# Performance work log

Hardware: AMD Instinct MI355X
Metric: run time of the kernel (lower is better)

Reference implementation:

```python
import jax, jax.numpy as jnp
import numpy as np

NUM_GROUPS = 128  # number of distinct values in min_t_idx (fixed for jit)


def _ball_volume(dim, radius):
    # dim is a static python int (NI - 1)
    if dim == 1:
        return 2.0 * radius
    if dim == 2:
        return jnp.pi * radius ** 2
    if dim == 3:
        return (4.0 / 3.0) * jnp.pi * radius ** 3
    raise ValueError(f'Only 1D-3D KDE volumes are supported, got dimension {dim}.')


def setup_inputs() -> dict:
    key = jax.random.key(0)
    k1, k2 = jax.random.split(key)
    M, NI = 16384, 3
    x = jax.random.normal(k1, (M, NI), dtype=jnp.float32)
    min_t_idx = jax.random.randint(k2, (M,), 0, NUM_GROUPS, dtype=jnp.int32)
    return {"x": x, "min_t_idx": min_t_idx, "K": 16}


def reference(x, min_t_idx, K):
    # Equivalent to the per-group python loop in the torch module, but done
    # densely: mask cross-group pairs to +inf and take the K-th smallest
    # distance per row (torch.kthvalue includes the self-distance 0, as here).
    M, NI = x.shape
    dim = NI - 1

    counts = jnp.bincount(min_t_idx, length=NUM_GROUPS)  # group sizes c
    c = counts[min_t_idx].astype(x.dtype)                # [M] size of own group (== N)

    # pairwise euclidean distances within groups
    sq = jnp.sum(x * x, axis=1)                          # [M]
    d2 = sq[:, None] + sq[None, :] - 2.0 * (x @ x.T)     # [M, M]
    dist = jnp.sqrt(jnp.maximum(d2, 0.0))
    same_group = min_t_idx[:, None] == min_t_idx[None, :]
    dist = jnp.where(same_group, dist, jnp.inf)

    # K-th smallest distance per row (includes self-distance 0)
    neg_topk, _ = jax.lax.top_k(-dist, K)                # [M, K]
    knn_dist = -neg_topk[:, K - 1]                       # [M]

    p_kde = _ball_volume(dim, knn_dist) / (K - 1)
    p_fallback = 1.0 / c                                 # groups with N < K
    p = jnp.where(c < K, p_fallback, p_kde)

    # original runs entirely under torch.no_grad()
    return jax.lax.stop_gradient(p)
```

## Files before the change

### kernel.cpp

```cpp
#include <hip/hip_runtime.h>
#include <hip/hip_bf16.h>
#include <float.h>

#define NGROUPS 128
#define SLOT    512
#define SB      512
#define RCAP    512


#define BUB(S) { const float lo_ = fminf(S, v); v = fmaxf(S, v); S = lo_; }

__global__ __launch_bounds__(SB) void kde_fused(
        const float* __restrict__ x,
        const int* __restrict__ idx,
        const int* __restrict__ Kptr,
        int M,
        float* __restrict__ out) {
    const int g = blockIdx.x >> 1;
    const int h = blockIdx.x & 1;

    __shared__ float4 cand[SLOT];
    __shared__ int    rows[RCAP];
    __shared__ float  Alds[2][64][17];
    __shared__ float  Blds[2][64][17];
    __shared__ int    lc, rc;

    const int tid  = threadIdx.x;
    const int wv   = tid >> 6;
    const int lane = tid & 63;

    if (tid == 0) { lc = 0; rc = 0; }
    __syncthreads();

    const int lo = h * (M >> 1);
    const int hi = lo + (M >> 1);

#define KDE_TRY(pid_)                                                         \
    do {                                                                      \
        const int pid = (pid_);                                               \
        int p = atomicAdd(&lc, 1);                                            \
        if (p < SLOT) {                                                       \
            float4 v;                                                         \
            v.x = x[3 * pid + 0];                                             \
            v.y = x[3 * pid + 1];                                             \
            v.z = x[3 * pid + 2];                                             \
            v.w = __int_as_float(pid);                                        \
            cand[p] = v;                                                      \
            if (pid >= lo && pid < hi) {                                      \
                int r = atomicAdd(&rc, 1);                                    \
                if (r < RCAP) rows[r] = p;                                    \
            }                                                                 \
        }                                                                     \
    } while (0)

    const int4* __restrict__ idx4 = (const int4*)idx;
    const int M4 = M >> 2;
    for (int i = tid; i < M4; i += SB) {
        const int4 v = idx4[i];
        const int base = i << 2;
        if (v.x == g) KDE_TRY(base + 0);
        if (v.y == g) KDE_TRY(base + 1);
        if (v.z == g) KDE_TRY(base + 2);
        if (v.w == g) KDE_TRY(base + 3);
    }
    for (int i = (M4 << 2) + tid; i < M; i += SB)
        if (idx[i] == g) KDE_TRY(i);
#undef KDE_TRY
    __syncthreads();

    int c  = lc;  c  = (c  < SLOT) ? c  : SLOT;
    int nr = rc;  nr = (nr < RCAP) ? nr : RCAP;
    const int K0 = Kptr[0];
    const int K  = (K0 < 16) ? K0 : 16;

    const int rg = wv >> 1;
    const int sp = wv & 1;

    const int ch = (c + 1) >> 1;
    const int j0 = sp ? ch : 0;
    const int j1 = sp ? c  : ch;

    for (int rbase = 0; rbase < nr; rbase += 128) {
        const bool grpActive = (wv < 4) && (rbase + rg * 64 < nr);
        const int  ridx      = rbase + rg * 64 + lane;
        const bool rowOK     = grpActive && (ridx < nr);
        int rslot = rowOK ? rows[ridx] : 0;
        rslot = (rslot >= 0 && rslot < SLOT) ? rslot : 0;
        const float4 rp = cand[rslot];

        float s0 = FLT_MAX, s1 = FLT_MAX, s2 = FLT_MAX, s3 = FLT_MAX;
        float s4 = FLT_MAX, s5 = FLT_MAX, s6 = FLT_MAX, s7 = FLT_MAX;
        float s8 = FLT_MAX, s9 = FLT_MAX, s10 = FLT_MAX, s11 = FLT_MAX;
        float s12 = FLT_MAX, s13 = FLT_MAX, s14 = FLT_MAX, s15 = FLT_MAX;

        if (grpActive) {
#pragma unroll 4
            for (int j = j0; j < j1; ++j) {
                const float4 q = cand[j];
                const float dx = q.x - rp.x;
                const float dy = q.y - rp.y;
                const float dz = q.z - rp.z;
                float v = dx * dx + dy * dy + dz * dz;
                BUB(s0)  BUB(s1)  BUB(s2)  BUB(s3)
                BUB(s4)  BUB(s5)  BUB(s6)  BUB(s7)
                BUB(s8)  BUB(s9)  BUB(s10) BUB(s11)
                BUB(s12) BUB(s13) BUB(s14) BUB(s15)
            }
            float (*dst)[17] = sp ? Blds[rg] : Alds[rg];
            dst[lane][0]  = s0;  dst[lane][1]  = s1;  dst[lane][2]  = s2;
            dst[lane][3]  = s3;  dst[lane][4]  = s4;  dst[lane][5]  = s5;
            dst[lane][6]  = s6;  dst[lane][7]  = s7;  dst[lane][8]  = s8;
            dst[lane][9]  = s9;  dst[lane][10] = s10; dst[lane][11] = s11;
            dst[lane][12] = s12; dst[lane][13] = s13; dst[lane][14] = s14;
            dst[lane][15] = s15;
        }
        __syncthreads();

        if (rowOK && sp == 0) {
            float kth;
            if (K == 16) {
                const float b0  = Blds[rg][lane][0],  b1  = Blds[rg][lane][1];
                const float b2  = Blds[rg][lane][2],  b3  = Blds[rg][lane][3];
                const float b4  = Blds[rg][lane][4],  b5  = Blds[rg][lane][5];
                const float b6  = Blds[rg][lane][6],  b7  = Blds[rg][lane][7];
                const float b8  = Blds[rg][lane][8],  b9  = Blds[rg][lane][9];
                const float b10 = Blds[rg][lane][10], b11 = Blds[rg][lane][11];
                const float b12 = Blds[rg][lane][12], b13 = Blds[rg][lane][13];
                const float b14 = Blds[rg][lane][14], b15 = Blds[rg][lane][15];
                float best = b15;
                best = fminf(best, fmaxf(s0,  b14));
                best = fminf(best, fmaxf(s1,  b13));
                best = fminf(best, fmaxf(s2,  b12));
                best = fminf(best, fmaxf(s3,  b11));
                best = fminf(best, fmaxf(s4,  b10));
                best = fminf(best, fmaxf(s5,  b9));
                best = fminf(best, fmaxf(s6,  b8));
                best = fminf(best, fmaxf(s7,  b7));
                best = fminf(best, fmaxf(s8,  b6));
                best = fminf(best, fmaxf(s9,  b5));
                best = fminf(best, fmaxf(s10, b4));
                best = fminf(best, fmaxf(s11, b3));
                best = fminf(best, fmaxf(s12, b2));
                best = fminf(best, fmaxf(s13, b1));
                best = fminf(best, fmaxf(s14, b0));
                best = fminf(best, s15);
                kth = best;
            } else {
                float best = FLT_MAX;
                for (int i = 0; i <= K; ++i) {
                    const float a = (i > 0)     ? Alds[rg][lane][i - 1]     : -FLT_MAX;
                    const float b = (K - i > 0) ? Blds[rg][lane][K - i - 1] : -FLT_MAX;
                    best = fminf(best, fmaxf(a, b));
                }
                kth = best;
            }
            const float pi = 3.14159265358979323846f;
            const float p = (c < K0) ? (1.0f / (float)c)
                                     : (pi * kth / (float)(K0 - 1));
            out[__float_as_int(rp.w)] = p;
        }
        __syncthreads();
    }
}

extern "C" void kernel_launch(void* const* d_in, const int* in_sizes, int n_in,
                              void* d_out, int out_size, void* d_ws, size_t ws_size,
                              hipStream_t stream) {
    const float* x   = (const float*)d_in[0];
    const int*   idx = (const int*)d_in[1];
    const int*   Kp  = (const int*)d_in[2];
    float* out = (float*)d_out;

    const int M = in_sizes[1];

    kde_fused<<<NGROUPS * 2, SB, 0, stream>>>(x, idx, Kp, M, out);
}
```

Baseline: 19.71 us.

## Split candidate scan across eight waves with bitonic tree merge of top-16 lists

Each row is now processed by all eight wavefronts, each scanning one eighth of the group's candidates, instead of two waves per row over half the candidates. The per-wave sorted top-16 lists are combined in a three-level tree through shared memory, using a bitonic min-merge so each merge stays sorted. This shortens the serial insertion-sort scan per thread, and every wave now does useful work instead of four idling. In exchange it adds three block barriers and extra merge ALU per 64-row batch, and rows are processed in batches of 64 rather than 128.

```diff
diff --git a/kernel.cpp b/kernel.cpp
--- a/kernel.cpp
+++ b/kernel.cpp
@@ -9,6 +9,7 @@
 
 
 #define BUB(S) { const float lo_ = fminf(S, v); v = fmaxf(S, v); S = lo_; }
+#define CS(a, b) { const float lo_ = fminf(a, b); b = fmaxf(a, b); a = lo_; }
 
 __global__ __launch_bounds__(SB) void kde_fused(
         const float* __restrict__ x,
@@ -21,8 +22,7 @@
 
     __shared__ float4 cand[SLOT];
     __shared__ int    rows[RCAP];
-    __shared__ float  Alds[2][64][17];
-    __shared__ float  Blds[2][64][17];
+    __shared__ float  lists[4][64][17];
     __shared__ int    lc, rc;
 
     const int tid  = threadIdx.x;
@@ -33,7 +33,7 @@
     __syncthreads();
 
     const int lo = h * (M >> 1);
-    const int hi = lo + (M >> 1);
+    const int hi = (h == 1) ? M : (M >> 1);
 
 #define KDE_TRY(pid_)                                                         \
     do {                                                                      \
@@ -71,93 +71,89 @@
     int c  = lc;  c  = (c  < SLOT) ? c  : SLOT;
     int nr = rc;  nr = (nr < RCAP) ? nr : RCAP;
     const int K0 = Kptr[0];
-    const int K  = (K0 < 16) ? K0 : 16;
 
-    const int rg = wv >> 1;
-    const int sp = wv & 1;
+    const int sh = (c + 7) >> 3;
+    const int j0 = wv * sh;
+    const int j1 = ((j0 + sh) < c) ? (j0 + sh) : c;
 
-    const int ch = (c + 1) >> 1;
-    const int j0 = sp ? ch : 0;
-    const int j1 = sp ? c  : ch;
+#define PUB(i)                                                                 \
+    do {                                                                       \
+        float* L = lists[i][lane];                                             \
+        L[0]=r0; L[1]=r1; L[2]=r2;  L[3]=r3;  L[4]=r4;  L[5]=r5;  L[6]=r6;     \
+        L[7]=r7; L[8]=r8; L[9]=r9;  L[10]=r10;L[11]=r11;L[12]=r12;L[13]=r13;   \
+        L[14]=r14; L[15]=r15;                                                  \
+    } while (0)
 
-    for (int rbase = 0; rbase < nr; rbase += 128) {
-        const bool grpActive = (wv < 4) && (rbase + rg * 64 < nr);
-        const int  ridx      = rbase + rg * 64 + lane;
-        const bool rowOK     = grpActive && (ridx < nr);
+#define MERGE16(i)                                                             \
+    do {                                                                       \
+        const float* L = lists[i][lane];                                       \
+        float m0  = fminf(r0,  L[15]); float m1  = fminf(r1,  L[14]);          \
+        float m2  = fminf(r2,  L[13]); float m3  = fminf(r3,  L[12]);          \
+        float m4  = fminf(r4,  L[11]); float m5  = fminf(r5,  L[10]);          \
+        float m6  = fminf(r6,  L[9]);  float m7  = fminf(r7,  L[8]);           \
+        float m8  = fminf(r8,  L[7]);  float m9  = fminf(r9,  L[6]);           \
+        float m10 = fminf(r10, L[5]);  float m11 = fminf(r11, L[4]);           \
+        float m12 = fminf(r12, L[3]);  float m13 = fminf(r13, L[2]);           \
+        float m14 = fminf(r14, L[1]);  float m15 = fminf(r15, L[0]);           \
+        CS(m0,m8)  CS(m1,m9)  CS(m2,m10) CS(m3,m11)                            \
+        CS(m4,m12) CS(m5,m13) CS(m6,m14) CS(m7,m15)                            \
+        CS(m0,m4)  CS(m1,m5)  CS(m2,m6)  CS(m3,m7)                             \
+        CS(m8,m12) CS(m9,m13) CS(m10,m14) CS(m11,m15)                          \
+        CS(m0,m2)  CS(m1,m3)  CS(m4,m6)  CS(m5,m7)                             \
+        CS(m8,m10) CS(m9,m11) CS(m12,m14) CS(m13,m15)                          \
+        CS(m0,m1)  CS(m2,m3)  CS(m4,m5)  CS(m6,m7)                             \
+        CS(m8,m9)  CS(m10,m11) CS(m12,m13) CS(m14,m15)                         \
+        r0=m0; r1=m1; r2=m2;  r3=m3;  r4=m4;  r5=m5;  r6=m6;  r7=m7;           \
+        r8=m8; r9=m9; r10=m10; r11=m11; r12=m12; r13=m13; r14=m14; r15=m15;    \
+    } while (0)
+
+    for (int rbase = 0; rbase < nr; rbase += 64) {
+        const int  ridx  = rbase + lane;
+        const bool rowOK = (ridx < nr);
         int rslot = rowOK ? rows[ridx] : 0;
         rslot = (rslot >= 0 && rslot < SLOT) ? rslot : 0;
         const float4 rp = cand[rslot];
 
-        float s0 = FLT_MAX, s1 = FLT_MAX, s2 = FLT_MAX, s3 = FLT_MAX;
-        float s4 = FLT_MAX, s5 = FLT_MAX, s6 = FLT_MAX, s7 = FLT_MAX;
-        float s8 = FLT_MAX, s9 = FLT_MAX, s10 = FLT_MAX, s11 = FLT_MAX;
-        float s12 = FLT_MAX, s13 = FLT_MAX, s14 = FLT_MAX, s15 = FLT_MAX;
+        float r0 = FLT_MAX, r1 = FLT_MAX, r2 = FLT_MAX, r3 = FLT_MAX;
+        float r4 = FLT_MAX, r5 = FLT_MAX, r6 = FLT_MAX, r7 = FLT_MAX;
+        float r8 = FLT_MAX, r9 = FLT_MAX, r10 = FLT_MAX, r11 = FLT_MAX;
+        float r12 = FLT_MAX, r13 = FLT_MAX, r14 = FLT_MAX, r15 = FLT_MAX;
 
-        if (grpActive) {
-#pragma unroll 4
-            for (int j = j0; j < j1; ++j) {
-                const float4 q = cand[j];
-                const float dx = q.x - rp.x;
-                const float dy = q.y - rp.y;
-                const float dz = q.z - rp.z;
-                float v = dx * dx + dy * dy + dz * dz;
-                BUB(s0)  BUB(s1)  BUB(s2)  BUB(s3)
-                BUB(s4)  BUB(s5)  BUB(s6)  BUB(s7)
-                BUB(s8)  BUB(s9)  BUB(s10) BUB(s11)
-                BUB(s12) BUB(s13) BUB(s14) BUB(s15)
+        for (int j = j0; j < j1; ++j) {
+            const float4 q = cand[j];
+            const float dx = q.x - rp.x;
+            const float dy = q.y - rp.y;
+            const float dz = q.z - rp.z;
+            float v = dx * dx + dy * dy + dz * dz;
+            BUB(r0)  BUB(r1)  BUB(r2)  BUB(r3)
+            BUB(r4)  BUB(r5)  BUB(r6)  BUB(r7)
+            BUB(r8)  BUB(r9)  BUB(r10) BUB(r11)
+            BUB(r12) BUB(r13) BUB(r14) BUB(r15)
+        }
+
+        if (wv >= 4) PUB(wv - 4);
+        __syncthreads();
+        if (wv < 4) MERGE16(wv);
+        if (wv == 2 || wv == 3) PUB(wv);
+        __syncthreads();
+        if (wv < 2) MERGE16(wv + 2);
+        if (wv == 1) PUB(1);
+        __syncthreads();
+        if (wv == 0) {
+            MERGE16(1);
+            if (rowOK) {
+                float kth;
+                if (K0 >= 16) {
+                    kth = r15;
+                } else {
+                    PUB(0);
+                    kth = lists[0][lane][K0 - 1];
+                }
+                const float pi = 3.14159265358979323846f;
+                const float p = (c < K0) ? (1.0f / (float)c)
+                                         : (pi * kth / (float)(K0 - 1));
+                out[__float_as_int(rp.w)] = p;
             }
-            float (*dst)[17] = sp ? Blds[rg] : Alds[rg];
-            dst[lane][0]  = s0;  dst[lane][1]  = s1;  dst[lane][2]  = s2;
-            dst[lane][3]  = s3;  dst[lane][4]  = s4;  dst[lane][5]  = s5;
-            dst[lane][6]  = s6;  dst[lane][7]  = s7;  dst[lane][8]  = s8;
-            dst[lane][9]  = s9;  dst[lane][10] = s10; dst[lane][11] = s11;
-            dst[lane][12] = s12; dst[lane][13] = s13; dst[lane][14] = s14;
-            dst[lane][15] = s15;
-        }
-        __syncthreads();
-
-        if (rowOK && sp == 0) {
-            float kth;
-            if (K == 16) {
-                const float b0  = Blds[rg][lane][0],  b1  = Blds[rg][lane][1];
-                const float b2  = Blds[rg][lane][2],  b3  = Blds[rg][lane][3];
-                const float b4  = Blds[rg][lane][4],  b5  = Blds[rg][lane][5];
-                const float b6  = Blds[rg][lane][6],  b7  = Blds[rg][lane][7];
-                const float b8  = Blds[rg][lane][8],  b9  = Blds[rg][lane][9];
-                const float b10 = Blds[rg][lane][10], b11 = Blds[rg][lane][11];
-                const float b12 = Blds[rg][lane][12], b13 = Blds[rg][lane][13];
-                const float b14 = Blds[rg][lane][14], b15 = Blds[rg][lane][15];
-                float best = b15;
-                best = fminf(best, fmaxf(s0,  b14));
-                best = fminf(best, fmaxf(s1,  b13));
-                best = fminf(best, fmaxf(s2,  b12));
-                best = fminf(best, fmaxf(s3,  b11));
-                best = fminf(best, fmaxf(s4,  b10));
-                best = fminf(best, fmaxf(s5,  b9));
-                best = fminf(best, fmaxf(s6,  b8));
-                best = fminf(best, fmaxf(s7,  b7));
-                best = fminf(best, fmaxf(s8,  b6));
-                best = fminf(best, fmaxf(s9,  b5));
-                best = fminf(best, fmaxf(s10, b4));
-                best = fminf(best, fmaxf(s11, b3));
-                best = fminf(best, fmaxf(s12, b2));
-                best = fminf(best, fmaxf(s13, b1));
-                best = fminf(best, fmaxf(s14, b0));
-                best = fminf(best, s15);
-                kth = best;
-            } else {
-                float best = FLT_MAX;
-                for (int i = 0; i <= K; ++i) {
-                    const float a = (i > 0)     ? Alds[rg][lane][i - 1]     : -FLT_MAX;
-                    const float b = (K - i > 0) ? Blds[rg][lane][K - i - 1] : -FLT_MAX;
-                    best = fminf(best, fmaxf(a, b));
-                }
-                kth = best;
-            }
-            const float pi = 3.14159265358979323846f;
-            const float p = (c < K0) ? (1.0f / (float)c)
-                                     : (pi * kth / (float)(K0 - 1));
-            out[__float_as_int(rp.w)] = p;
         }
         __syncthreads();
     }
```

New measurement: 24.10 us. 22.2% more time.
